# Performance work log

Measured on AMD Instinct MI355X. Metric: run time of the kernel, lower is better.

The kernel has to match this reference:

```python
import jax, jax.numpy as jnp
import numpy as np

E2M1_GRID = jnp.array([0.0, 0.5, 1.0, 1.5, 2.0, 3.0, 4.0, 6.0], dtype=jnp.float32)
E2M1_MIDS = (E2M1_GRID[1:] + E2M1_GRID[:-1]) / 2.0
FP4_MAX = 6.0
FP8_E4M3_MAX = 448.0


def nvfp4_quant_dequant(w):
    # Emulates tetrajetv2.quant_fp4_dequant_trans_fused: two-level scaling
    # (fp32 outer scale per 128 inputs, fp8-e4m3 inner scale per 16 inputs),
    # values rounded to the signed E2M1 grid, then dequantized.
    O, I = w.shape
    w16 = w.reshape(O, I // 128, 8, 16)
    amax128 = jnp.max(jnp.abs(w16), axis=(-2, -1))          # [O, I/128]
    outer = amax128 / (FP4_MAX * FP8_E4M3_MAX)
    outer = jnp.where(outer > 0, outer, 1.0)
    amax16 = jnp.max(jnp.abs(w16), axis=-1)                  # [O, I/128, 8]
    inner = amax16 / FP4_MAX / outer[..., None]
    inner = inner.astype(jnp.float8_e4m3fn).astype(jnp.float32)  # fp8 round
    scale = outer[..., None] * inner                          # [O, I/128, 8]
    safe = jnp.where(scale > 0, scale, 1.0)[..., None]
    code = w16 / safe
    a = jnp.abs(code)
    idx = jnp.searchsorted(E2M1_MIDS, a)                      # nearest grid pt
    q = E2M1_GRID[idx] * jnp.sign(code)
    return (q * scale[..., None]).reshape(O, I)


def setup_inputs() -> dict:
    key = jax.random.key(0)
    k0, k1, k2 = jax.random.split(key, 3)
    B, S, H = 2, 2048, 2048
    hidden_states = jax.random.normal(k0, (B, S, H), dtype=jnp.float32)
    # raw weights ~ N(0, 0.023) as in FP4Linear init, then fake-quantized
    w_qkv = jax.random.normal(k1, (3 * H, H), dtype=jnp.float32) * 0.023
    w_o = jax.random.normal(k2, (H, H), dtype=jnp.float32) * 0.023
    w_qkv = nvfp4_quant_dequant(w_qkv)
    w_o = nvfp4_quant_dequant(w_o)
    return {"hidden_states": hidden_states, "w_qkv": w_qkv, "w_o": w_o}


def reference(hidden_states, w_qkv, w_o):
    B, S, H = hidden_states.shape
    num_heads = 16
    head_dim = H // num_heads
    qkv = jnp.einsum('bsh,oh->bso', hidden_states, w_qkv)      # [B,S,3H]
    qkv = qkv.reshape(B, S, 3, num_heads, head_dim)
    qkv = jnp.transpose(qkv, (2, 0, 3, 1, 4))                  # [3,B,nh,S,hd]
    q, k, v = qkv[0], qkv[1], qkv[2]
    scale = 1.0 / jnp.sqrt(jnp.float32(head_dim))
    scores = jnp.einsum('bhqd,bhkd->bhqk', q, k) * scale
    causal = jnp.tril(jnp.ones((S, S), dtype=bool))
    scores = jnp.where(causal, scores, jnp.finfo(scores.dtype).min)
    probs = jax.nn.softmax(scores, axis=-1)
    attn = jnp.einsum('bhqk,bhkd->bhqd', probs, v)             # [B,nh,S,hd]
    attn = jnp.transpose(attn, (0, 2, 1, 3)).reshape(B, S, H)
    return jnp.einsum('bsh,oh->bso', attn, w_o)
```

## Files before the change

### kernel.cpp

```cpp
#include <hip/hip_runtime.h>
#include <hip/hip_bf16.h>
#include <stdint.h>

typedef __bf16 bf16x8 __attribute__((ext_vector_type(8)));
typedef float f32x4 __attribute__((ext_vector_type(4)));

#define AS1 __attribute__((address_space(1)))
#define AS3 __attribute__((address_space(3)))

#define PBAR() do { __builtin_amdgcn_sched_barrier(0); asm volatile("s_barrier" ::: "memory"); __builtin_amdgcn_sched_barrier(0); } while (0)
#define LGK0() do { asm volatile("s_waitcnt lgkmcnt(0)" ::: "memory"); __builtin_amdgcn_sched_barrier(0); } while (0)
#define VMCNT(n) do { asm volatile("s_waitcnt vmcnt(" #n ")" ::: "memory"); __builtin_amdgcn_sched_barrier(0); } while (0)

__device__ __forceinline__ unsigned short f2bf(float x) {
    union { float f; uint32_t u; } v; v.f = x;
    uint32_t r = v.u + 0x7fffu + ((v.u >> 16) & 1u);
    return (unsigned short)(r >> 16);
}

__global__ void k_f2bf(const float* __restrict__ in, unsigned short* __restrict__ out, int n4) {
    int i = blockIdx.x * blockDim.x + threadIdx.x;
    if (i >= n4) return;
    float4 v = reinterpret_cast<const float4*>(in)[i];
    ushort4 o;
    o.x = f2bf(v.x); o.y = f2bf(v.y); o.z = f2bf(v.z); o.w = f2bf(v.w);
    reinterpret_cast<ushort4*>(out)[i] = o;
}

template <typename TOUT>
__global__ __launch_bounds__(512, 2) void k_gemm128x256(
    const unsigned short* __restrict__ A,
    const unsigned short* __restrict__ B,
    TOUT* __restrict__ C, int M, int N, int K, int ngrid)
{
    __shared__ __align__(16) unsigned short Albuf[3][4096];
    __shared__ __align__(16) unsigned short Blbuf[3][8192];
    const int tid = threadIdx.x, lane = tid & 63, wv = tid >> 6;
    const int wr = wv >> 2, wc = wv & 3;
    const int fl = lane & 15, fg = lane >> 4;
    const int cpx = ngrid >> 3;
    const int sw = ((int)blockIdx.x & 7) * cpx + ((int)blockIdx.x >> 3);
    const int bm = sw & 31, bn = sw >> 5;
    const int nK = K >> 5;

    const unsigned short* Ag = A + (size_t)bm * 128 * K;
    const unsigned short* Bg = B + (size_t)bn * 256 * K;

    auto stageA = [&](int buf, int t) {
        const int r = tid >> 2;
        const int cs = (tid & 3) ^ ((r >> 1) & 3);
        const unsigned short* src = Ag + (size_t)r * K + t * 32 + cs * 8;
        __builtin_amdgcn_global_load_lds((const AS1 void*)src,
            (AS3 void*)((char*)&Albuf[buf][0] + wv * 1024), 16, 0, 0);
    };
    auto stageB = [&](int buf, int half, int t) {
        const int r = tid >> 2;
        const int cs = (tid & 3) ^ ((r >> 1) & 3);
        const unsigned short* src = Bg + (size_t)(half * 128 + r) * K + t * 32 + cs * 8;
        __builtin_amdgcn_global_load_lds((const AS1 void*)src,
            (AS3 void*)((char*)&Blbuf[buf][0] + half * 8192 + wv * 1024), 16, 0, 0);
    };
    auto ldfrag = [&](const unsigned short* base, int r) -> bf16x8 {
        return *reinterpret_cast<const bf16x8*>(
            (const char*)base + r * 64 + ((fg ^ ((r >> 1) & 3)) << 4));
    };

    f32x4 acc[4][4];
#pragma unroll
    for (int i = 0; i < 4; ++i)
#pragma unroll
        for (int j = 0; j < 4; ++j) acc[i][j] = (f32x4){0.f, 0.f, 0.f, 0.f};

    stageA(0, 0); stageB(0, 0, 0); stageB(0, 1, 0);
    stageA(1, 1); stageB(1, 0, 1); stageB(1, 1, 1);
    asm volatile("s_waitcnt vmcnt(3)" ::: "memory");
    PBAR();

    int c = 0;
    for (int t = 0; t < nK; ++t) {
        const unsigned short* Ac = Albuf[c];
        const unsigned short* Bc = Blbuf[c];
        bf16x8 af[4], bv[4];
#pragma unroll
        for (int i = 0; i < 4; ++i) af[i] = ldfrag(Ac, wr * 64 + i * 16 + fl);
#pragma unroll
        for (int j = 0; j < 4; ++j) bv[j] = ldfrag(Bc, wc * 64 + j * 16 + fl);
        if (t + 2 < nK) {
            int nb = c + 2; if (nb >= 3) nb -= 3;
            stageA(nb, t + 2); stageB(nb, 0, t + 2); stageB(nb, 1, t + 2);
        }
        PBAR();
        LGK0();
        __builtin_amdgcn_s_setprio(1);
#pragma unroll
        for (int i = 0; i < 4; ++i)
#pragma unroll
            for (int j = 0; j < 4; ++j)
                acc[i][j] = __builtin_amdgcn_mfma_f32_16x16x32_bf16(af[i], bv[j], acc[i][j], 0, 0, 0);
        __builtin_amdgcn_s_setprio(0);
        if (t + 2 < nK)      { asm volatile("s_waitcnt vmcnt(3)" ::: "memory"); }
        else if (t + 1 < nK) { asm volatile("s_waitcnt vmcnt(0)" ::: "memory"); }
        PBAR();
        ++c; if (c == 3) c = 0;
    }

#pragma unroll
    for (int i = 0; i < 4; ++i)
#pragma unroll
        for (int j = 0; j < 4; ++j)
#pragma unroll
            for (int r = 0; r < 4; ++r) {
                int row = bm * 128 + wr * 64 + i * 16 + fg * 4 + r;
                int col = bn * 256 + wc * 64 + j * 16 + fl;
                float v = acc[i][j][r];
                if constexpr (sizeof(TOUT) == 2)
                    ((unsigned short*)C)[(size_t)row * N + col] = f2bf(v);
                else
                    C[(size_t)row * N + col] = v;
            }
}

__global__ void k_transpose_v(const unsigned short* __restrict__ qkv, unsigned short* __restrict__ vT) {
    __shared__ unsigned short t[32][33];
    const int bh = blockIdx.z;
    const int b = bh >> 4, h = bh & 15;
    const int s0 = blockIdx.x * 32, d0 = blockIdx.y * 32;
    const int tx = threadIdx.x, ty = threadIdx.y;
#pragma unroll
    for (int i = 0; i < 4; ++i) {
        int s = s0 + ty + i * 8;
        t[ty + i * 8][tx] = qkv[(size_t)(b * 2048 + s) * 6144 + 4096 + h * 128 + d0 + tx];
    }
    __syncthreads();
#pragma unroll
    for (int i = 0; i < 4; ++i) {
        int d = d0 + ty + i * 8;
        vT[((size_t)bh * 128 + d) * 2048 + s0 + tx] = t[tx][ty + i * 8];
    }
}

__global__ __launch_bounds__(256, 2) void k_attn(
    const unsigned short* __restrict__ qkv, const unsigned short* __restrict__ vT,
    unsigned short* __restrict__ out)
{
    __shared__ unsigned short Klds[2][8192];
    __shared__ unsigned short Vlds[8192];
    __shared__ __align__(16) unsigned short Plds[4][2048];

    const int tid = threadIdx.x, lane = tid & 63, wv = tid >> 6;
    const int fl = lane & 15, fg = lane >> 4;
    const int bh = blockIdx.y;
    const int qb = (bh >= 16) ? blockIdx.x : 15 - blockIdx.x;
    const int b = bh >> 4, h = bh & 15;
    const int q0w = qb * 128 + wv * 32;
    const size_t base = (size_t)b * 2048 * 6144 + (size_t)h * 128;
    const unsigned short* Qbase = qkv + base;
    const unsigned short* Kbase = qkv + base + 2048;
    const unsigned short* Vbase = vT + (size_t)bh * 128 * 2048;
    unsigned short* pw = Plds[wv];

    bf16x8 qf[2][4];
#pragma unroll
    for (int m = 0; m < 2; ++m)
#pragma unroll
        for (int kk = 0; kk < 4; ++kk)
            qf[m][kk] = *reinterpret_cast<const bf16x8*>(
                Qbase + (size_t)(q0w + m * 16 + fl) * 6144 + kk * 32 + fg * 8);
    asm volatile("s_waitcnt vmcnt(0)" ::: "memory");
    __builtin_amdgcn_sched_barrier(0);

    auto stageK = [&](int buf, int kv0) {
#pragma unroll
        for (int rnd = 0; rnd < 4; ++rnd) {
            int ch = rnd * 256 + tid;
            int row = ch >> 4;
            int cbl = ((ch & 15) << 4) ^ ((row & 7) << 4);
            const unsigned short* src = Kbase + (size_t)(kv0 + row) * 6144 + (cbl >> 1);
            __builtin_amdgcn_global_load_lds((const AS1 void*)src,
                (AS3 void*)((char*)&Klds[buf][0] + (rnd * 256 + wv * 64) * 16), 16, 0, 0);
        }
    };
    auto stageV = [&](int kv0) {
#pragma unroll
        for (int rnd = 0; rnd < 4; ++rnd) {
            int ch = rnd * 256 + tid;
            int row = ch >> 3;
            int cbl = ((ch & 7) << 4) ^ ((row & 7) << 4);
            const unsigned short* src = Vbase + (size_t)row * 2048 + kv0 + (cbl >> 1);
            __builtin_amdgcn_global_load_lds((const AS1 void*)src,
                (AS3 void*)((char*)&Vlds[0] + (rnd * 256 + wv * 64) * 16), 16, 0, 0);
        }
    };

    f32x4 acc[2][8];
#pragma unroll
    for (int m = 0; m < 2; ++m)
#pragma unroll
        for (int nb = 0; nb < 8; ++nb) acc[m][nb] = (f32x4){0.f, 0.f, 0.f, 0.f};
    float l_r[2] = {0.f, 0.f};
    const float sc = 0.08838834764831845f;
    const int nIter = 2 * qb + 2;

    stageK(0, 0);

    for (int it = 0; it < nIter; ++it) {
        const int kv0 = it * 64;
        const bool act = (kv0 <= q0w + 31);
        const bool haveK = (it + 1 < nIter);
        stageV(kv0);
        if (haveK) stageK((it + 1) & 1, kv0 + 64);
        __builtin_amdgcn_sched_barrier(0);
        if (haveK) { VMCNT(8); } else { VMCNT(4); }
        PBAR();
        if (act) {
            const bool full = (kv0 + 63 <= q0w);
            const unsigned short* Kb = Klds[it & 1];
            f32x4 s[2][4];
#pragma unroll
            for (int m = 0; m < 2; ++m)
#pragma unroll
                for (int n = 0; n < 4; ++n) s[m][n] = (f32x4){0.f, 0.f, 0.f, 0.f};
            __builtin_amdgcn_s_setprio(1);
#pragma unroll
            for (int kk = 0; kk < 4; ++kk)
#pragma unroll
                for (int n = 0; n < 4; ++n) {
                    const int row = n * 16 + fl;
                    bf16x8 kf = *reinterpret_cast<const bf16x8*>(
                        (const char*)Kb + row * 256 + ((kk * 64 + fg * 16) ^ ((row & 7) << 4)));
                    s[0][n] = __builtin_amdgcn_mfma_f32_16x16x32_bf16(kf, qf[0][kk], s[0][n], 0, 0, 0);
                    s[1][n] = __builtin_amdgcn_mfma_f32_16x16x32_bf16(kf, qf[1][kk], s[1][n], 0, 0, 0);
                }
            __builtin_amdgcn_s_setprio(0);
#pragma unroll
            for (int m = 0; m < 2; ++m) {
                const int qi = q0w + m * 16 + fl;
                const int prow = m * 16 + fl;
                const int rb = prow * 128, swz = (prow & 7) << 4;
#pragma unroll
                for (int n = 0; n < 4; ++n) {
                    const int kbase = kv0 + n * 16 + fg * 4;
                    float v0 = s[m][n][0] * sc, v1 = s[m][n][1] * sc,
                          v2 = s[m][n][2] * sc, v3 = s[m][n][3] * sc;
                    if (!full) {
                        if (kbase     > qi) v0 = -3e38f;
                        if (kbase + 1 > qi) v1 = -3e38f;
                        if (kbase + 2 > qi) v2 = -3e38f;
                        if (kbase + 3 > qi) v3 = -3e38f;
                    }
                    float p0 = __expf(v0 - 10.f), p1 = __expf(v1 - 10.f),
                          p2 = __expf(v2 - 10.f), p3 = __expf(v3 - 10.f);
                    l_r[m] += p0 + p1 + p2 + p3;
                    uint32_t lo = (uint32_t)f2bf(p0) | ((uint32_t)f2bf(p1) << 16);
                    uint32_t hi = (uint32_t)f2bf(p2) | ((uint32_t)f2bf(p3) << 16);
                    const int byte = rb + ((n * 32 + fg * 8) ^ swz);
                    uint2 pk; pk.x = lo; pk.y = hi;
                    *reinterpret_cast<uint2*>((char*)pw + byte) = pk;
                }
            }
            LGK0();
        }
        if (haveK) { VMCNT(4); } else { VMCNT(0); }
        PBAR();
        if (act) {
            bf16x8 pf[2][2];
#pragma unroll
            for (int m = 0; m < 2; ++m)
#pragma unroll
                for (int k2 = 0; k2 < 2; ++k2) {
                    const int row = m * 16 + fl;
                    pf[m][k2] = *reinterpret_cast<const bf16x8*>(
                        (const char*)pw + row * 128 + ((k2 * 64 + fg * 16) ^ ((row & 7) << 4)));
                }
            __builtin_amdgcn_s_setprio(1);
#pragma unroll
            for (int nb = 0; nb < 8; ++nb)
#pragma unroll
                for (int k2 = 0; k2 < 2; ++k2) {
                    const int d = nb * 16 + fl;
                    bf16x8 vf = *reinterpret_cast<const bf16x8*>(
                        (const char*)Vlds + d * 128 + ((k2 * 64 + fg * 16) ^ ((d & 7) << 4)));
                    acc[0][nb] = __builtin_amdgcn_mfma_f32_16x16x32_bf16(pf[0][k2], vf, acc[0][nb], 0, 0, 0);
                    acc[1][nb] = __builtin_amdgcn_mfma_f32_16x16x32_bf16(pf[1][k2], vf, acc[1][nb], 0, 0, 0);
                }
            __builtin_amdgcn_s_setprio(0);
        }
        PBAR();
    }

#pragma unroll
    for (int m = 0; m < 2; ++m) {
        float l = l_r[m];
        l += __shfl_xor(l, 16);
        l += __shfl_xor(l, 32);
        float inv[4];
#pragma unroll
        for (int r = 0; r < 4; ++r) inv[r] = 1.0f / __shfl(l, fg * 4 + r);
#pragma unroll
        for (int nb = 0; nb < 8; ++nb)
#pragma unroll
            for (int r = 0; r < 4; ++r) {
                int row = q0w + m * 16 + fg * 4 + r;
                int col = h * 128 + nb * 16 + fl;
                out[(size_t)(b * 2048 + row) * 2048 + col] = f2bf(acc[m][nb][r] * inv[r]);
            }
    }
}

extern "C" void kernel_launch(void* const* d_in, const int* in_sizes, int n_in,
                              void* d_out, int out_size, void* d_ws, size_t ws_size,
                              hipStream_t stream) {
    const float* hs   = (const float*)d_in[0];
    const float* wqkv = (const float*)d_in[1];
    const float* wo   = (const float*)d_in[2];
    float* out = (float*)d_out;

    char* p = (char*)d_ws;
    unsigned short* Xb    = (unsigned short*)p; p += (size_t)4096 * 2048 * 2;
    unsigned short* Wqkvb = (unsigned short*)p; p += (size_t)6144 * 2048 * 2;
    unsigned short* Wob   = (unsigned short*)p; p += (size_t)2048 * 2048 * 2;
    unsigned short* QKV   = (unsigned short*)p; p += (size_t)4096 * 6144 * 2;
    unsigned short* VT    = (unsigned short*)p; p += (size_t)32 * 128 * 2048 * 2;
    unsigned short* ATTN  = (unsigned short*)p; p += (size_t)4096 * 2048 * 2;

    k_f2bf<<<8192, 256, 0, stream>>>(hs, Xb, 2097152);
    k_f2bf<<<12288, 256, 0, stream>>>(wqkv, Wqkvb, 3145728);
    k_f2bf<<<4096, 256, 0, stream>>>(wo, Wob, 1048576);
    k_gemm128x256<unsigned short><<<768, 512, 0, stream>>>(Xb, Wqkvb, QKV, 4096, 6144, 2048, 768);
    k_transpose_v<<<dim3(64, 4, 32), dim3(32, 8), 0, stream>>>(QKV, VT);
    k_attn<<<dim3(16, 32), 256, 0, stream>>>(QKV, VT, ATTN);
    k_gemm128x256<float><<<256, 512, 0, stream>>>(ATTN, Wob, out, 4096, 2048, 2048, 256);
}
```

Before: 263.0 us.

## Use 256x256 tile GEMM with double buffering for QKV projection

```diff
diff --git a/kernel.cpp b/kernel.cpp
--- a/kernel.cpp
+++ b/kernel.cpp
@@ -25,6 +25,90 @@
     ushort4 o;
     o.x = f2bf(v.x); o.y = f2bf(v.y); o.z = f2bf(v.z); o.w = f2bf(v.w);
     reinterpret_cast<ushort4*>(out)[i] = o;
+}
+
+__global__ __launch_bounds__(512, 2) void k_gemm256x256(
+    const unsigned short* __restrict__ A,
+    const unsigned short* __restrict__ B,
+    unsigned short* __restrict__ C, int M, int N, int K, int ngrid)
+{
+    __shared__ __align__(16) unsigned short Al[2][8192];
+    __shared__ __align__(16) unsigned short Bl[2][8192];
+    const int tid = threadIdx.x, lane = tid & 63, wv = tid >> 6;
+    const int wr = wv >> 2, wc = wv & 3;
+    const int fl = lane & 15, fg = lane >> 4;
+    const int cpx = ngrid >> 3;
+    const int sw = ((int)blockIdx.x & 7) * cpx + ((int)blockIdx.x >> 3);
+    const int bm = sw & 15, bn = sw >> 4;
+    const int nK = K >> 5;
+
+    const unsigned short* Ag = A + (size_t)bm * 256 * K;
+    const unsigned short* Bg = B + (size_t)bn * 256 * K;
+
+    auto stage = [&](int buf, int t) {
+#pragma unroll
+        for (int u = 0; u < 2; ++u) {
+            int ch = u * 512 + tid;
+            int r = ch >> 2, cs = (ch & 3) ^ ((r >> 1) & 3);
+            __builtin_amdgcn_global_load_lds(
+                (const AS1 void*)(Ag + (size_t)r * K + t * 32 + cs * 8),
+                (AS3 void*)((char*)&Al[buf][0] + ch * 16), 16, 0, 0);
+        }
+#pragma unroll
+        for (int u = 0; u < 2; ++u) {
+            int ch = u * 512 + tid;
+            int r = ch >> 2, cs = (ch & 3) ^ ((r >> 1) & 3);
+            __builtin_amdgcn_global_load_lds(
+                (const AS1 void*)(Bg + (size_t)r * K + t * 32 + cs * 8),
+                (AS3 void*)((char*)&Bl[buf][0] + ch * 16), 16, 0, 0);
+        }
+    };
+    auto ldfrag = [&](const unsigned short* base, int r) -> bf16x8 {
+        return *reinterpret_cast<const bf16x8*>(
+            (const char*)base + r * 64 + ((fg ^ ((r >> 1) & 3)) << 4));
+    };
+
+    f32x4 acc[8][4];
+#pragma unroll
+    for (int i = 0; i < 8; ++i)
+#pragma unroll
+        for (int j = 0; j < 4; ++j) acc[i][j] = (f32x4){0.f, 0.f, 0.f, 0.f};
+
+    stage(0, 0);
+    VMCNT(0);
+    PBAR();
+
+    for (int t = 0; t < nK; ++t) {
+        const int c = t & 1;
+        if (t + 1 < nK) stage(c ^ 1, t + 1);
+        __builtin_amdgcn_sched_barrier(0);
+        bf16x8 af[8], bv[4];
+#pragma unroll
+        for (int i = 0; i < 8; ++i) af[i] = ldfrag(Al[c], wr * 128 + i * 16 + fl);
+#pragma unroll
+        for (int j = 0; j < 4; ++j) bv[j] = ldfrag(Bl[c], wc * 64 + j * 16 + fl);
+        LGK0();
+        __builtin_amdgcn_s_setprio(1);
+#pragma unroll
+        for (int i = 0; i < 8; ++i)
+#pragma unroll
+            for (int j = 0; j < 4; ++j)
+                acc[i][j] = __builtin_amdgcn_mfma_f32_16x16x32_bf16(af[i], bv[j], acc[i][j], 0, 0, 0);
+        __builtin_amdgcn_s_setprio(0);
+        if (t + 1 < nK) { VMCNT(0); }
+        PBAR();
+    }
+
+#pragma unroll
+    for (int i = 0; i < 8; ++i)
+#pragma unroll
+        for (int j = 0; j < 4; ++j)
+#pragma unroll
+            for (int r = 0; r < 4; ++r) {
+                int row = bm * 256 + wr * 128 + i * 16 + fg * 4 + r;
+                int col = bn * 256 + wc * 64 + j * 16 + fl;
+                C[(size_t)row * N + col] = f2bf(acc[i][j][r]);
+            }
 }
 
 template <typename TOUT>
@@ -326,7 +410,7 @@
     k_f2bf<<<8192, 256, 0, stream>>>(hs, Xb, 2097152);
     k_f2bf<<<12288, 256, 0, stream>>>(wqkv, Wqkvb, 3145728);
     k_f2bf<<<4096, 256, 0, stream>>>(wo, Wob, 1048576);
-    k_gemm128x256<unsigned short><<<768, 512, 0, stream>>>(Xb, Wqkvb, QKV, 4096, 6144, 2048, 768);
+    k_gemm256x256<<<384, 512, 0, stream>>>(Xb, Wqkvb, QKV, 4096, 6144, 2048, 384);
     k_transpose_v<<<dim3(64, 4, 32), dim3(32, 8), 0, stream>>>(QKV, VT);
     k_attn<<<dim3(16, 32), 256, 0, stream>>>(QKV, VT, ATTN);
     k_gemm128x256<float><<<256, 512, 0, stream>>>(ATTN, Wob, out, 4096, 2048, 2048, 256);
```

Result: slower. 301.3 us (+14.6%).
